# Performance work log

Hardware: AMD Instinct MI355X
Metric: run time of the kernel (lower is better)

Reference implementation:

```python
import jax, jax.numpy as jnp
import numpy as np
from jax import lax

DIM = 1024
B, N = 4, 4096


def setup_inputs() -> dict:
    key = jax.random.key(0)
    k1, k2 = jax.random.split(key)
    x = jax.random.normal(k1, (B, N, DIM), dtype=jnp.float32)
    # Linear(dim, 3*dim, bias=False): weight stored as [3*dim, dim] (torch convention)
    w_qkva = jax.random.normal(k2, (3 * DIM, DIM), dtype=jnp.float32) * (DIM ** -0.5)
    gamma = jnp.ones((DIM,), dtype=jnp.float32)  # RMSNorm gain
    return {"x": x, "w_qkva": w_qkva, "gamma": gamma}


def _rmsnorm(x, gamma):
    # lucidrains RMSNorm: F.normalize(x, dim=-1) * sqrt(dim) * gamma
    scale = jnp.asarray(x.shape[-1], x.dtype) ** 0.5
    norm = jnp.sqrt(jnp.sum(x * x, axis=-1, keepdims=True))
    return x / jnp.maximum(norm, 1e-12) * scale * gamma


def reference(x, w_qkva, gamma):
    h = _rmsnorm(x, gamma)                                  # [b, n, d]
    qkva = jnp.einsum('bnd,ed->bne', h, w_qkva)             # [b, n, 3d]
    q, kv, a = jnp.split(qkva, 3, axis=-1)                  # each [b, n, d]
    a = jax.nn.sigmoid(a)

    def binary_operator(e_i, e_j):
        a_i, kv_i = e_i
        a_j, kv_j = e_j
        return (a_j * a_i, a_j * kv_i + kv_j)

    # gated linear recurrence over the sequence axis (elementwise per channel)
    _, y = lax.associative_scan(binary_operator, (a, kv), axis=1)
    return q * y                                            # [b, n, d]
```

## Files before the change

### kernel.cpp

```cpp
#include <hip/hip_runtime.h>
#include <hip/hip_bf16.h>

#define SEQ_N 4096
#define BATCH 4
#define DIM 1024
#define M_ROWS (BATCH * SEQ_N)
#define NCOLS (3 * DIM)
#define KDIM DIM
#define CHUNK_L 64
#define NCHUNK (SEQ_N / CHUNK_L)
#define NCHANNEL (BATCH * DIM)

using short8 = __attribute__((ext_vector_type(8))) short;
using f32x4  = __attribute__((ext_vector_type(4))) float;

static __device__ __forceinline__ unsigned short f2bf(float f) {
    union { float f; unsigned u; } v; v.f = f;
    unsigned r = v.u + 0x7fffu + ((v.u >> 16) & 1u);
    return (unsigned short)(r >> 16);
}
static __device__ __forceinline__ float bf2f(unsigned short s) {
    union { unsigned u; float f; } v; v.u = ((unsigned)s) << 16;
    return v.f;
}

__global__ __launch_bounds__(256) void wconv_kernel(const float* __restrict__ in,
                                                    unsigned short* __restrict__ out,
                                                    int n4) {
    int i = blockIdx.x * 256 + threadIdx.x;
    if (i < n4) {
        float4 v = reinterpret_cast<const float4*>(in)[i];
        ushort4 o;
        o.x = f2bf(v.x); o.y = f2bf(v.y); o.z = f2bf(v.z); o.w = f2bf(v.w);
        reinterpret_cast<ushort4*>(out)[i] = o;
    }
}

__global__ __launch_bounds__(256) void rmsnorm_kernel(const float* __restrict__ x,
                                                      const float* __restrict__ gamma,
                                                      unsigned short* __restrict__ h) {
    const int row = blockIdx.x;
    const int tid = threadIdx.x;
    const float4 v = reinterpret_cast<const float4*>(x + (size_t)row * DIM)[tid];
    float ss = v.x * v.x + v.y * v.y + v.z * v.z + v.w * v.w;
#pragma unroll
    for (int off = 32; off >= 1; off >>= 1) ss += __shfl_xor(ss, off, 64);
    __shared__ float red[4];
    if ((tid & 63) == 0) red[tid >> 6] = ss;
    __syncthreads();
    const float tot = red[0] + red[1] + red[2] + red[3];
    const float scale = 32.0f / fmaxf(sqrtf(tot), 1e-12f);
    const float4 g = reinterpret_cast<const float4*>(gamma)[tid];
    ushort4 o;
    o.x = f2bf(v.x * scale * g.x);
    o.y = f2bf(v.y * scale * g.y);
    o.z = f2bf(v.z * scale * g.z);
    o.w = f2bf(v.w * scale * g.w);
    reinterpret_cast<ushort4*>(h + (size_t)row * DIM)[tid] = o;
}

__global__ __launch_bounds__(256) void gemm_bt_kernel(const unsigned short* __restrict__ A,
                                                      const unsigned short* __restrict__ B,
                                                      unsigned short* __restrict__ C) {
    __shared__ __align__(16) unsigned short sA[128 * 32];
    __shared__ __align__(16) unsigned short sB[128 * 32];

    const int tid  = threadIdx.x;
    const int lane = tid & 63;
    const int wave = tid >> 6;
    const int row0 = blockIdx.y * 128;
    const int col0 = blockIdx.x * 128;
    const int wm = (wave >> 1) * 64;
    const int wn = (wave & 1) * 64;
    const int fr = lane & 15;
    const int kq = lane >> 4;

    const unsigned short* agp = A + (size_t)(row0 + (tid >> 2)) * KDIM + (tid & 3) * 8;
    const unsigned short* bgp = B + (size_t)(col0 + (tid >> 2)) * KDIM + (tid & 3) * 8;

    f32x4 acc[4][4] = {};

    for (int k0 = 0; k0 < KDIM; k0 += 32) {
        __builtin_amdgcn_global_load_lds(
            (const __attribute__((address_space(1))) void*)(agp),
            (__attribute__((address_space(3))) void*)(&sA[tid * 8]), 16, 0, 0);
        __builtin_amdgcn_global_load_lds(
            (const __attribute__((address_space(1))) void*)(agp + 64 * KDIM),
            (__attribute__((address_space(3))) void*)(&sA[2048 + tid * 8]), 16, 0, 0);
        __builtin_amdgcn_global_load_lds(
            (const __attribute__((address_space(1))) void*)(bgp),
            (__attribute__((address_space(3))) void*)(&sB[tid * 8]), 16, 0, 0);
        __builtin_amdgcn_global_load_lds(
            (const __attribute__((address_space(1))) void*)(bgp + 64 * KDIM),
            (__attribute__((address_space(3))) void*)(&sB[2048 + tid * 8]), 16, 0, 0);
        agp += 32; bgp += 32;
        __syncthreads();

        short8 af[4], bf[4];
#pragma unroll
        for (int i = 0; i < 4; ++i)
            af[i] = *reinterpret_cast<const short8*>(&sA[(wm + i * 16 + fr) * 32 + kq * 8]);
#pragma unroll
        for (int j = 0; j < 4; ++j)
            bf[j] = *reinterpret_cast<const short8*>(&sB[(wn + j * 16 + fr) * 32 + kq * 8]);
#pragma unroll
        for (int i = 0; i < 4; ++i)
#pragma unroll
            for (int j = 0; j < 4; ++j)
                acc[i][j] = __builtin_amdgcn_mfma_f32_16x16x32_bf16(bf[j], af[i], acc[i][j], 0, 0, 0);
        __syncthreads();
    }

#pragma unroll
    for (int i = 0; i < 4; ++i) {
        const size_t rbase = (size_t)(row0 + wm + i * 16 + fr) * NCOLS;
#pragma unroll
        for (int j = 0; j < 4; ++j) {
            const int col = col0 + wn + j * 16 + kq * 4;
            ushort4 o;
            o.x = f2bf(acc[i][j][0]);
            o.y = f2bf(acc[i][j][1]);
            o.z = f2bf(acc[i][j][2]);
            o.w = f2bf(acc[i][j][3]);
            *reinterpret_cast<ushort4*>(&C[rbase + col]) = o;
        }
    }
}

__global__ __launch_bounds__(128) void chunk_agg_kernel(const unsigned short* __restrict__ qkva,
                                                        float* __restrict__ Aagg,
                                                        float* __restrict__ Yagg) {
    const int c = blockIdx.x, b = blockIdx.z;
    const int d4 = blockIdx.y * 128 + threadIdx.x;
    const unsigned short* base = qkva + ((size_t)b * SEQ_N + c * CHUNK_L) * NCOLS;
    float s[4] = {0.f, 0.f, 0.f, 0.f};
    float A[4] = {1.f, 1.f, 1.f, 1.f};
#pragma unroll 4
    for (int n = 0; n < CHUNK_L; ++n) {
        ushort4 kv4 = reinterpret_cast<const ushort4*>(base + (size_t)n * NCOLS + DIM)[d4];
        ushort4 av4 = reinterpret_cast<const ushort4*>(base + (size_t)n * NCOLS + 2 * DIM)[d4];
        float kv[4] = {bf2f(kv4.x), bf2f(kv4.y), bf2f(kv4.z), bf2f(kv4.w)};
        float av[4] = {bf2f(av4.x), bf2f(av4.y), bf2f(av4.z), bf2f(av4.w)};
#pragma unroll
        for (int t = 0; t < 4; ++t) {
            float a = 1.f / (1.f + __expf(-av[t]));
            s[t] = a * s[t] + kv[t];
            A[t] *= a;
        }
    }
    float4 Ao, Yo;
    Ao.x = A[0]; Ao.y = A[1]; Ao.z = A[2]; Ao.w = A[3];
    Yo.x = s[0]; Yo.y = s[1]; Yo.z = s[2]; Yo.w = s[3];
    reinterpret_cast<float4*>(Aagg + c * NCHANNEL + b * DIM)[d4 & 255] = Ao;
    reinterpret_cast<float4*>(Yagg + c * NCHANNEL + b * DIM)[d4 & 255] = Yo;
}

__global__ __launch_bounds__(256) void agg_scan_kernel(const float* __restrict__ Aagg,
                                                       const float* __restrict__ Yagg,
                                                       float* __restrict__ Sin) {
    const int ch = blockIdx.x * 256 + threadIdx.x;
    float s = 0.f;
#pragma unroll 4
    for (int c = 0; c < NCHUNK; ++c) {
        Sin[c * NCHANNEL + ch] = s;
        s = Aagg[c * NCHANNEL + ch] * s + Yagg[c * NCHANNEL + ch];
    }
}

__global__ __launch_bounds__(128) void apply_kernel(const unsigned short* __restrict__ qkva,
                                                    const float* __restrict__ Sin,
                                                    float* __restrict__ out) {
    const int c = blockIdx.x, b = blockIdx.z;
    const int d4 = blockIdx.y * 128 + threadIdx.x;
    const unsigned short* base = qkva + ((size_t)b * SEQ_N + c * CHUNK_L) * NCOLS;
    float* obase = out + ((size_t)b * SEQ_N + c * CHUNK_L) * DIM;
    float4 s4 = reinterpret_cast<const float4*>(Sin + c * NCHANNEL + b * DIM)[d4 & 255];
    float s[4] = {s4.x, s4.y, s4.z, s4.w};
#pragma unroll 4
    for (int n = 0; n < CHUNK_L; ++n) {
        ushort4 kv4 = reinterpret_cast<const ushort4*>(base + (size_t)n * NCOLS + DIM)[d4];
        ushort4 av4 = reinterpret_cast<const ushort4*>(base + (size_t)n * NCOLS + 2 * DIM)[d4];
        ushort4 q4  = reinterpret_cast<const ushort4*>(base + (size_t)n * NCOLS)[d4];
        float kv[4] = {bf2f(kv4.x), bf2f(kv4.y), bf2f(kv4.z), bf2f(kv4.w)};
        float av[4] = {bf2f(av4.x), bf2f(av4.y), bf2f(av4.z), bf2f(av4.w)};
        float q[4]  = {bf2f(q4.x),  bf2f(q4.y),  bf2f(q4.z),  bf2f(q4.w)};
        float4 o;
        {
            float a0 = 1.f / (1.f + __expf(-av[0])); s[0] = a0 * s[0] + kv[0]; o.x = q[0] * s[0];
            float a1 = 1.f / (1.f + __expf(-av[1])); s[1] = a1 * s[1] + kv[1]; o.y = q[1] * s[1];
            float a2 = 1.f / (1.f + __expf(-av[2])); s[2] = a2 * s[2] + kv[2]; o.z = q[2] * s[2];
            float a3 = 1.f / (1.f + __expf(-av[3])); s[3] = a3 * s[3] + kv[3]; o.w = q[3] * s[3];
        }
        reinterpret_cast<float4*>(obase + (size_t)n * DIM)[d4] = o;
    }
}

extern "C" void kernel_launch(void* const* d_in, const int* in_sizes, int n_in,
                              void* d_out, int out_size, void* d_ws, size_t ws_size,
                              hipStream_t stream) {
    const float* x     = (const float*)d_in[0];
    const float* w     = (const float*)d_in[1];
    const float* gamma = (const float*)d_in[2];
    float* out = (float*)d_out;

    char* ws = (char*)d_ws;
    unsigned short* wb   = (unsigned short*)(ws);
    unsigned short* h    = (unsigned short*)(ws + 6291456);
    unsigned short* qkva = (unsigned short*)(ws + 39845888);
    float* Aagg = (float*)(ws + 140509184);
    float* Yagg = (float*)(ws + 141557760);
    float* Sin  = (float*)(ws + 142606336);

    wconv_kernel<<<(NCOLS * KDIM / 4 + 255) / 256, 256, 0, stream>>>(w, wb, NCOLS * KDIM / 4);
    rmsnorm_kernel<<<M_ROWS, 256, 0, stream>>>(x, gamma, h);
    gemm_bt_kernel<<<dim3(NCOLS / 128, M_ROWS / 128), 256, 0, stream>>>(h, wb, qkva);
    chunk_agg_kernel<<<dim3(NCHUNK, 2, BATCH), 128, 0, stream>>>(qkva, Aagg, Yagg);
    agg_scan_kernel<<<NCHANNEL / 256, 256, 0, stream>>>(Aagg, Yagg, Sin);
    apply_kernel<<<dim3(NCHUNK, 2, BATCH), 128, 0, stream>>>(qkva, Sin, out);
}
```

Measured before the change: 321.8 us.

## Shrink scan chunks, widen scan blocks, change GEMM output layout, reuse workspace

The scan chunk length drops from 64 to 16, which gives four times as many chunks, and the chunk and apply kernels now use 256-thread blocks covering the full channel width. The per-chunk serial work gets shorter and there are more blocks to run in parallel, but agg_scan_kernel now walks 256 chunks serially. The GEMM swaps the MFMA operand order and writes scalar bf16 values instead of vectorized ushort4 stores, which is likely slower for the output write. The aggregate buffers are moved to reuse the workspace region of the normalized activations h, which is no longer needed once the GEMM has run.

After: 307.9 us. 4.3% less time.

```diff
diff --git a/kernel.cpp b/kernel.cpp
--- a/kernel.cpp
+++ b/kernel.cpp
@@ -7,7 +7,7 @@
 #define M_ROWS (BATCH * SEQ_N)
 #define NCOLS (3 * DIM)
 #define KDIM DIM
-#define CHUNK_L 64
+#define CHUNK_L 16
 #define NCHUNK (SEQ_N / CHUNK_L)
 #define NCHANNEL (BATCH * DIM)
 
@@ -107,31 +107,29 @@
         for (int i = 0; i < 4; ++i)
 #pragma unroll
             for (int j = 0; j < 4; ++j)
-                acc[i][j] = __builtin_amdgcn_mfma_f32_16x16x32_bf16(bf[j], af[i], acc[i][j], 0, 0, 0);
+                acc[i][j] = __builtin_amdgcn_mfma_f32_16x16x32_bf16(af[i], bf[j], acc[i][j], 0, 0, 0);
         __syncthreads();
     }
 
 #pragma unroll
     for (int i = 0; i < 4; ++i) {
-        const size_t rbase = (size_t)(row0 + wm + i * 16 + fr) * NCOLS;
 #pragma unroll
         for (int j = 0; j < 4; ++j) {
-            const int col = col0 + wn + j * 16 + kq * 4;
-            ushort4 o;
-            o.x = f2bf(acc[i][j][0]);
-            o.y = f2bf(acc[i][j][1]);
-            o.z = f2bf(acc[i][j][2]);
-            o.w = f2bf(acc[i][j][3]);
-            *reinterpret_cast<ushort4*>(&C[rbase + col]) = o;
+#pragma unroll
+            for (int r = 0; r < 4; ++r) {
+                int row = row0 + wm + i * 16 + kq * 4 + r;
+                int col = col0 + wn + j * 16 + fr;
+                C[(size_t)row * NCOLS + col] = f2bf(acc[i][j][r]);
+            }
         }
     }
 }
 
-__global__ __launch_bounds__(128) void chunk_agg_kernel(const unsigned short* __restrict__ qkva,
+__global__ __launch_bounds__(256) void chunk_agg_kernel(const unsigned short* __restrict__ qkva,
                                                         float* __restrict__ Aagg,
                                                         float* __restrict__ Yagg) {
-    const int c = blockIdx.x, b = blockIdx.z;
-    const int d4 = blockIdx.y * 128 + threadIdx.x;
+    const int c = blockIdx.x, b = blockIdx.y;
+    const int d4 = threadIdx.x;
     const unsigned short* base = qkva + ((size_t)b * SEQ_N + c * CHUNK_L) * NCOLS;
     float s[4] = {0.f, 0.f, 0.f, 0.f};
     float A[4] = {1.f, 1.f, 1.f, 1.f};
@@ -151,8 +149,8 @@
     float4 Ao, Yo;
     Ao.x = A[0]; Ao.y = A[1]; Ao.z = A[2]; Ao.w = A[3];
     Yo.x = s[0]; Yo.y = s[1]; Yo.z = s[2]; Yo.w = s[3];
-    reinterpret_cast<float4*>(Aagg + c * NCHANNEL + b * DIM)[d4 & 255] = Ao;
-    reinterpret_cast<float4*>(Yagg + c * NCHANNEL + b * DIM)[d4 & 255] = Yo;
+    reinterpret_cast<float4*>(Aagg + (size_t)c * NCHANNEL + b * DIM)[d4] = Ao;
+    reinterpret_cast<float4*>(Yagg + (size_t)c * NCHANNEL + b * DIM)[d4] = Yo;
 }
 
 __global__ __launch_bounds__(256) void agg_scan_kernel(const float* __restrict__ Aagg,
@@ -160,21 +158,21 @@
                                                        float* __restrict__ Sin) {
     const int ch = blockIdx.x * 256 + threadIdx.x;
     float s = 0.f;
-#pragma unroll 4
+#pragma unroll 8
     for (int c = 0; c < NCHUNK; ++c) {
-        Sin[c * NCHANNEL + ch] = s;
-        s = Aagg[c * NCHANNEL + ch] * s + Yagg[c * NCHANNEL + ch];
-    }
-}
-
-__global__ __launch_bounds__(128) void apply_kernel(const unsigned short* __restrict__ qkva,
+        Sin[(size_t)c * NCHANNEL + ch] = s;
+        s = Aagg[(size_t)c * NCHANNEL + ch] * s + Yagg[(size_t)c * NCHANNEL + ch];
+    }
+}
+
+__global__ __launch_bounds__(256) void apply_kernel(const unsigned short* __restrict__ qkva,
                                                     const float* __restrict__ Sin,
                                                     float* __restrict__ out) {
-    const int c = blockIdx.x, b = blockIdx.z;
-    const int d4 = blockIdx.y * 128 + threadIdx.x;
+    const int c = blockIdx.x, b = blockIdx.y;
+    const int d4 = threadIdx.x;
     const unsigned short* base = qkva + ((size_t)b * SEQ_N + c * CHUNK_L) * NCOLS;
     float* obase = out + ((size_t)b * SEQ_N + c * CHUNK_L) * DIM;
-    float4 s4 = reinterpret_cast<const float4*>(Sin + c * NCHANNEL + b * DIM)[d4 & 255];
+    float4 s4 = reinterpret_cast<const float4*>(Sin + (size_t)c * NCHANNEL + b * DIM)[d4];
     float s[4] = {s4.x, s4.y, s4.z, s4.w};
 #pragma unroll 4
     for (int n = 0; n < CHUNK_L; ++n) {
@@ -207,14 +205,14 @@
     unsigned short* wb   = (unsigned short*)(ws);
     unsigned short* h    = (unsigned short*)(ws + 6291456);
     unsigned short* qkva = (unsigned short*)(ws + 39845888);
-    float* Aagg = (float*)(ws + 140509184);
-    float* Yagg = (float*)(ws + 141557760);
-    float* Sin  = (float*)(ws + 142606336);
+    float* Aagg = (float*)(ws + 6291456);
+    float* Yagg = (float*)(ws + 6291456 + 4194304);
+    float* Sin  = (float*)(ws + 6291456 + 8388608);
 
     wconv_kernel<<<(NCOLS * KDIM / 4 + 255) / 256, 256, 0, stream>>>(w, wb, NCOLS * KDIM / 4);
     rmsnorm_kernel<<<M_ROWS, 256, 0, stream>>>(x, gamma, h);
     gemm_bt_kernel<<<dim3(NCOLS / 128, M_ROWS / 128), 256, 0, stream>>>(h, wb, qkva);
-    chunk_agg_kernel<<<dim3(NCHUNK, 2, BATCH), 128, 0, stream>>>(qkva, Aagg, Yagg);
+    chunk_agg_kernel<<<dim3(NCHUNK, BATCH), 256, 0, stream>>>(qkva, Aagg, Yagg);
     agg_scan_kernel<<<NCHANNEL / 256, 256, 0, stream>>>(Aagg, Yagg, Sin);
-    apply_kernel<<<dim3(NCHUNK, 2, BATCH), 128, 0, stream>>>(qkva, Sin, out);
-}
+    apply_kernel<<<dim3(NCHUNK, BATCH), 256, 0, stream>>>(qkva, Sin, out);
+}
```
